# Optimization experiments

Measured on AMD Instinct MI355X. Metric: run time of the kernel, lower is better.

Reference implementation:

```python
import jax, jax.numpy as jnp
import numpy as np

HIDDEN = 1024
VOCAB = 50257
N_LAYERS = 2


def setup_inputs() -> dict:
    key = jax.random.key(0)
    ks = jax.random.split(key, 8)
    s = 1.0 / np.sqrt(HIDDEN)
    inp = {
        "input_id": jax.random.randint(ks[0], (1,), 0, VOCAB, dtype=jnp.int64)
        if jax.config.jax_enable_x64 else jax.random.randint(ks[0], (1,), 0, VOCAB, dtype=jnp.int32),
        "h0": jnp.zeros((1, 1, HIDDEN), jnp.float32),
        "c0": jnp.zeros((1, 1, HIDDEN), jnp.float32),
        "emb": jax.random.normal(ks[1], (VOCAB, HIDDEN), jnp.float32),
        # PyTorch LSTM gate order: i, f, g, o stacked along first dim (4H, H)
        "W_ih": jax.random.uniform(ks[2], (4 * HIDDEN, HIDDEN), jnp.float32, -s, s),
        "W_hh": jax.random.uniform(ks[3], (4 * HIDDEN, HIDDEN), jnp.float32, -s, s),
        "b_ih": jax.random.uniform(ks[4], (4 * HIDDEN,), jnp.float32, -s, s),
        "b_hh": jax.random.uniform(ks[5], (4 * HIDDEN,), jnp.float32, -s, s),
        "W_out": jax.random.uniform(ks[6], (VOCAB, HIDDEN), jnp.float32, -s, s),
        "b_out": jax.random.uniform(ks[7], (VOCAB,), jnp.float32, -s, s),
    }
    return inp


def _lstm_step(x, h, c, W_ih, W_hh, b_ih, b_hh):
    # x, h, c: [1, H]; gates: [1, 4H] in torch order i, f, g, o
    gates = x @ W_ih.T + b_ih + h @ W_hh.T + b_hh
    i, f, g, o = jnp.split(gates, 4, axis=-1)
    c_new = jax.nn.sigmoid(f) * c + jax.nn.sigmoid(i) * jnp.tanh(g)
    h_new = jax.nn.sigmoid(o) * jnp.tanh(c_new)
    return h_new, c_new


def reference(input_id, h0, c0, emb, W_ih, W_hh, b_ih, b_hh, W_out, b_out):
    # embedding(input).view(1,1,-1) -> treat as [1, H] (seq=1, batch=1)
    x = emb[input_id[0]][None, :]            # [1, H]
    h = h0[0]                                # [1, H]
    c = c0[0]                                # [1, H]
    for _ in range(N_LAYERS):                # re-applies the SAME lstm, as in source
        x = jax.nn.relu(x)
        h, c = _lstm_step(x, h, c, W_ih, W_hh, b_ih, b_hh)
        x = h
    logits = x @ W_out.T + b_out             # [1, VOCAB]
    out = jax.nn.log_softmax(logits, axis=-1)
    return out, (h[None], c[None])
```

## Files before the change

kernel.cpp:

```cpp
#include <hip/hip_runtime.h>
#include <math.h>

#define HID 1024
#define VOCABN 50257

__device__ __forceinline__ float dot4(float4 a, float4 b) {
    return a.x * b.x + a.y * b.y + a.z * b.z + a.w * b.w;
}

__device__ __forceinline__ float sigmoidf(float x) {
    return 1.f / (1.f + expf(-x));
}

__global__ __launch_bounds__(256) void lstm_layer_kernel(
    const float* __restrict__ x_src, const int* __restrict__ idx, int use_idx,
    const float* __restrict__ h_in, const float* __restrict__ c_in,
    const float* __restrict__ W_ih, const float* __restrict__ W_hh,
    const float* __restrict__ b_ih, const float* __restrict__ b_hh,
    float* __restrict__ h_out, float* __restrict__ c_out)
{
    const int u = blockIdx.x;
    const int t = threadIdx.x;

    const float* x = x_src;
    if (use_idx) x += (size_t)(*idx) * HID;

    float4 xv = reinterpret_cast<const float4*>(x)[t];
    xv.x = fmaxf(xv.x, 0.f); xv.y = fmaxf(xv.y, 0.f);
    xv.z = fmaxf(xv.z, 0.f); xv.w = fmaxf(xv.w, 0.f);
    float4 hv = reinterpret_cast<const float4*>(h_in)[t];

    float acc[8];
#pragma unroll
    for (int g = 0; g < 4; ++g) {
        const float4* wi = reinterpret_cast<const float4*>(W_ih + (size_t)(g * HID + u) * HID);
        const float4* wh = reinterpret_cast<const float4*>(W_hh + (size_t)(g * HID + u) * HID);
        acc[g]     = dot4(wi[t], xv);
        acc[4 + g] = dot4(wh[t], hv);
    }

#pragma unroll
    for (int off = 32; off > 0; off >>= 1) {
#pragma unroll
        for (int g = 0; g < 8; ++g) acc[g] += __shfl_down(acc[g], off);
    }

    __shared__ float red[4][8];
    const int wave = t >> 6, lane = t & 63;
    if (lane == 0) {
#pragma unroll
        for (int g = 0; g < 8; ++g) red[wave][g] = acc[g];
    }
    __syncthreads();

    if (t == 0) {
        float s[8];
#pragma unroll
        for (int g = 0; g < 8; ++g)
            s[g] = red[0][g] + red[1][g] + red[2][g] + red[3][g];
        float gi = s[0] + s[4] + b_ih[u]           + b_hh[u];
        float gf = s[1] + s[5] + b_ih[HID + u]     + b_hh[HID + u];
        float gg = s[2] + s[6] + b_ih[2 * HID + u] + b_hh[2 * HID + u];
        float go = s[3] + s[7] + b_ih[3 * HID + u] + b_hh[3 * HID + u];
        float i_ = sigmoidf(gi);
        float f_ = sigmoidf(gf);
        float g_ = tanhf(gg);
        float o_ = sigmoidf(go);
        float cn = f_ * c_in[u] + i_ * g_;
        float hn = o_ * tanhf(cn);
        h_out[u] = hn;
        c_out[u] = cn;
    }
}

__global__ __launch_bounds__(256) void logits_kernel(
    const float* __restrict__ xh, const float* __restrict__ W_out,
    const float* __restrict__ b_out, float* __restrict__ logits)
{
    const int wave = threadIdx.x >> 6, lane = threadIdx.x & 63;
    const int v = blockIdx.x * 4 + wave;
    if (v >= VOCABN) return;

    const float4* w  = reinterpret_cast<const float4*>(W_out + (size_t)v * HID);
    const float4* x4 = reinterpret_cast<const float4*>(xh);
    float acc = 0.f;
#pragma unroll
    for (int j = 0; j < 4; ++j) {
        const int k = lane + j * 64;
        acc += dot4(w[k], x4[k]);
    }
#pragma unroll
    for (int off = 32; off > 0; off >>= 1) acc += __shfl_down(acc, off);
    if (lane == 0) logits[v] = acc + b_out[v];
}

__global__ __launch_bounds__(1024) void lse_kernel(
    const float* __restrict__ logits, float* __restrict__ lse)
{
    const int t = threadIdx.x;
    float m = -1e30f, s = 0.f;
    for (int i = t; i < VOCABN; i += 1024) {
        float v = logits[i];
        if (v > m) { s = s * expf(m - v) + 1.f; m = v; }
        else       { s += expf(v - m); }
    }
#pragma unroll
    for (int off = 32; off > 0; off >>= 1) {
        float m2 = __shfl_down(m, off), s2 = __shfl_down(s, off);
        float mn = fmaxf(m, m2);
        s = s * expf(m - mn) + s2 * expf(m2 - mn);
        m = mn;
    }
    __shared__ float ms[16], ss[16];
    const int wave = t >> 6, lane = t & 63;
    if (lane == 0) { ms[wave] = m; ss[wave] = s; }
    __syncthreads();
    if (t == 0) {
        float M = ms[0], S = ss[0];
#pragma unroll
        for (int w = 1; w < 16; ++w) {
            float mn = fmaxf(M, ms[w]);
            S = S * expf(M - mn) + ss[w] * expf(ms[w] - mn);
            M = mn;
        }
        *lse = M + logf(S);
    }
}

__global__ __launch_bounds__(256) void finalize_kernel(
    const float* __restrict__ logits, const float* __restrict__ lse,
    float* __restrict__ out)
{
    const int i = blockIdx.x * 256 + threadIdx.x;
    if (i < VOCABN) out[i] = logits[i] - *lse;
}

extern "C" void kernel_launch(void* const* d_in, const int* in_sizes, int n_in,
                              void* d_out, int out_size, void* d_ws, size_t ws_size,
                              hipStream_t stream) {
    const int*   idx   = (const int*)d_in[0];
    const float* h0    = (const float*)d_in[1];
    const float* c0    = (const float*)d_in[2];
    const float* emb   = (const float*)d_in[3];
    const float* W_ih  = (const float*)d_in[4];
    const float* W_hh  = (const float*)d_in[5];
    const float* b_ih  = (const float*)d_in[6];
    const float* b_hh  = (const float*)d_in[7];
    const float* W_out = (const float*)d_in[8];
    const float* b_out = (const float*)d_in[9];

    float* out = (float*)d_out;
    float* h_final = out + VOCABN;
    float* c_final = out + VOCABN + HID;

    float* ws     = (float*)d_ws;
    float* h1     = ws;
    float* c1     = ws + HID;
    float* logits = ws + 2 * HID;
    float* lse    = ws + 2 * HID + VOCABN;

    lstm_layer_kernel<<<HID, 256, 0, stream>>>(emb, idx, 1, h0, c0,
                                               W_ih, W_hh, b_ih, b_hh, h1, c1);
    lstm_layer_kernel<<<HID, 256, 0, stream>>>(h1, nullptr, 0, h1, c1,
                                               W_ih, W_hh, b_ih, b_hh, h_final, c_final);
    logits_kernel<<<(VOCABN + 3) / 4, 256, 0, stream>>>(h_final, W_out, b_out, logits);
    lse_kernel<<<1, 1024, 0, stream>>>(logits, lse);
    finalize_kernel<<<(VOCABN + 255) / 256, 256, 0, stream>>>(logits, lse, out);
}
```

Measured before the change: 419.7 us.

## Fuse log-sum-exp partials into logits kernel and drop single-block LSE pass

The logits kernel now has each wave compute four vocabulary rows, reusing the hidden vector held in registers. Each block also emits a partial (max, sum-exp) pair to workspace. The serial single-block LSE kernel is removed. Every finalize block instead reduces all per-block partials itself before subtracting the log-sum-exp, which trades one launch and a slow single-block pass for redundant small reductions across blocks.

Result: faster. 409.9 us (-2.3%).

```diff
diff --git a/kernel.cpp b/kernel.cpp
--- a/kernel.cpp
+++ b/kernel.cpp
@@ -3,12 +3,14 @@
 
 #define HID 1024
 #define VOCABN 50257
+#define ROWS_PER_BLOCK 16
+#define NLOGB ((VOCABN + ROWS_PER_BLOCK - 1) / ROWS_PER_BLOCK)
 
 __device__ __forceinline__ float dot4(float4 a, float4 b) {
     return a.x * b.x + a.y * b.y + a.z * b.z + a.w * b.w;
 }
 
-__device__ __forceinline__ float sigmoidf(float x) {
+__device__ __forceinline__ float sigmoidf_(float x) {
     return 1.f / (1.f + expf(-x));
 }
 
@@ -62,10 +64,10 @@
         float gf = s[1] + s[5] + b_ih[HID + u]     + b_hh[HID + u];
         float gg = s[2] + s[6] + b_ih[2 * HID + u] + b_hh[2 * HID + u];
         float go = s[3] + s[7] + b_ih[3 * HID + u] + b_hh[3 * HID + u];
-        float i_ = sigmoidf(gi);
-        float f_ = sigmoidf(gf);
+        float i_ = sigmoidf_(gi);
+        float f_ = sigmoidf_(gf);
         float g_ = tanhf(gg);
-        float o_ = sigmoidf(go);
+        float o_ = sigmoidf_(go);
         float cn = f_ * c_in[u] + i_ * g_;
         float hn = o_ * tanhf(cn);
         h_out[u] = hn;
@@ -75,34 +77,75 @@
 
 __global__ __launch_bounds__(256) void logits_kernel(
     const float* __restrict__ xh, const float* __restrict__ W_out,
-    const float* __restrict__ b_out, float* __restrict__ logits)
+    const float* __restrict__ b_out, float* __restrict__ logits,
+    float2* __restrict__ partials)
 {
     const int wave = threadIdx.x >> 6, lane = threadIdx.x & 63;
-    const int v = blockIdx.x * 4 + wave;
-    if (v >= VOCABN) return;
-
-    const float4* w  = reinterpret_cast<const float4*>(W_out + (size_t)v * HID);
+    const int vbase = blockIdx.x * ROWS_PER_BLOCK + wave * 4;
+
     const float4* x4 = reinterpret_cast<const float4*>(xh);
-    float acc = 0.f;
-#pragma unroll
-    for (int j = 0; j < 4; ++j) {
-        const int k = lane + j * 64;
-        acc += dot4(w[k], x4[k]);
-    }
-#pragma unroll
-    for (int off = 32; off > 0; off >>= 1) acc += __shfl_down(acc, off);
-    if (lane == 0) logits[v] = acc + b_out[v];
-}
-
-__global__ __launch_bounds__(1024) void lse_kernel(
-    const float* __restrict__ logits, float* __restrict__ lse)
+    float4 xr[4];
+#pragma unroll
+    for (int j = 0; j < 4; ++j) xr[j] = x4[lane + j * 64];
+
+    float acc[4];
+#pragma unroll
+    for (int r = 0; r < 4; ++r) {
+        const int v = vbase + r;
+        float a = 0.f;
+        if (v < VOCABN) {
+            const float4* w = reinterpret_cast<const float4*>(W_out + (size_t)v * HID);
+#pragma unroll
+            for (int j = 0; j < 4; ++j) a += dot4(w[lane + j * 64], xr[j]);
+        }
+        acc[r] = a;
+    }
+#pragma unroll
+    for (int off = 32; off > 0; off >>= 1) {
+#pragma unroll
+        for (int r = 0; r < 4; ++r) acc[r] += __shfl_down(acc[r], off);
+    }
+
+    __shared__ float2 wred[4];
+    if (lane == 0) {
+        float m = -1e30f, s = 0.f;
+#pragma unroll
+        for (int r = 0; r < 4; ++r) {
+            const int v = vbase + r;
+            if (v < VOCABN) {
+                float L = acc[r] + b_out[v];
+                logits[v] = L;
+                if (L > m) { s = s * expf(m - L) + 1.f; m = L; }
+                else       { s += expf(L - m); }
+            }
+        }
+        wred[wave] = make_float2(m, s);
+    }
+    __syncthreads();
+    if (threadIdx.x == 0) {
+        float M = wred[0].x, S = wred[0].y;
+#pragma unroll
+        for (int w = 1; w < 4; ++w) {
+            float m2 = wred[w].x, s2 = wred[w].y;
+            float mn = fmaxf(M, m2);
+            S = S * expf(M - mn) + s2 * expf(m2 - mn);
+            M = mn;
+        }
+        partials[blockIdx.x] = make_float2(M, S);
+    }
+}
+
+__global__ __launch_bounds__(256) void finalize_kernel(
+    const float* __restrict__ logits, const float2* __restrict__ partials,
+    float* __restrict__ out)
 {
     const int t = threadIdx.x;
     float m = -1e30f, s = 0.f;
-    for (int i = t; i < VOCABN; i += 1024) {
-        float v = logits[i];
-        if (v > m) { s = s * expf(m - v) + 1.f; m = v; }
-        else       { s += expf(v - m); }
+    for (int i = t; i < NLOGB; i += 256) {
+        float2 p = partials[i];
+        float mn = fmaxf(m, p.x);
+        s = s * expf(m - mn) + p.y * expf(p.x - mn);
+        m = mn;
     }
 #pragma unroll
     for (int off = 32; off > 0; off >>= 1) {
@@ -111,28 +154,25 @@
         s = s * expf(m - mn) + s2 * expf(m2 - mn);
         m = mn;
     }
-    __shared__ float ms[16], ss[16];
+    __shared__ float ms[4], ss[4];
+    __shared__ float lse_sh;
     const int wave = t >> 6, lane = t & 63;
     if (lane == 0) { ms[wave] = m; ss[wave] = s; }
     __syncthreads();
     if (t == 0) {
         float M = ms[0], S = ss[0];
 #pragma unroll
-        for (int w = 1; w < 16; ++w) {
+        for (int w = 1; w < 4; ++w) {
             float mn = fmaxf(M, ms[w]);
             S = S * expf(M - mn) + ss[w] * expf(ms[w] - mn);
             M = mn;
         }
-        *lse = M + logf(S);
-    }
-}
-
-__global__ __launch_bounds__(256) void finalize_kernel(
-    const float* __restrict__ logits, const float* __restrict__ lse,
-    float* __restrict__ out)
-{
-    const int i = blockIdx.x * 256 + threadIdx.x;
-    if (i < VOCABN) out[i] = logits[i] - *lse;
+        lse_sh = M + logf(S);
+    }
+    __syncthreads();
+    const float lse = lse_sh;
+    const int i = blockIdx.x * 256 + t;
+    if (i < VOCABN) out[i] = logits[i] - lse;
 }
 
 extern "C" void kernel_launch(void* const* d_in, const int* in_sizes, int n_in,
@@ -153,17 +193,16 @@
     float* h_final = out + VOCABN;
     float* c_final = out + VOCABN + HID;
 
-    float* ws     = (float*)d_ws;
-    float* h1     = ws;
-    float* c1     = ws + HID;
-    float* logits = ws + 2 * HID;
-    float* lse    = ws + 2 * HID + VOCABN;
+    float*  ws       = (float*)d_ws;
+    float*  h1       = ws;
+    float*  c1       = ws + HID;
+    float*  logits   = ws + 2 * HID;
+    float2* partials = (float2*)(ws + 2 * HID + VOCABN + 1);
 
     lstm_layer_kernel<<<HID, 256, 0, stream>>>(emb, idx, 1, h0, c0,
                                                W_ih, W_hh, b_ih, b_hh, h1, c1);
     lstm_layer_kernel<<<HID, 256, 0, stream>>>(h1, nullptr, 0, h1, c1,
                                                W_ih, W_hh, b_ih, b_hh, h_final, c_final);
-    logits_kernel<<<(VOCABN + 3) / 4, 256, 0, stream>>>(h_final, W_out, b_out, logits);
-    lse_kernel<<<1, 1024, 0, stream>>>(logits, lse);
-    finalize_kernel<<<(VOCABN + 255) / 256, 256, 0, stream>>>(logits, lse, out);
-}
+    logits_kernel<<<NLOGB, 256, 0, stream>>>(h_final, W_out, b_out, logits, partials);
+    finalize_kernel<<<(VOCABN + 255) / 256, 256, 0, stream>>>(logits, partials, out);
+}
```
